# Kernel optimization log

Measured on AMD Instinct MI355X. Metric: run time of the kernel, lower is better.

The kernel has to match this reference:

```python
import jax, jax.numpy as jnp
import numpy as np

DIM = 180
HEADS = 6
WH, WW = 8, 8
MLP_HIDDEN = 720
EPS = 1e-5


def _rel_pos_index(wh, ww):
    ch = np.arange(wh)
    cw = np.arange(ww)
    coords = np.stack(np.meshgrid(ch, cw, indexing='ij'))  # [2, wh, ww]
    cf = coords.reshape(2, -1)                              # [2, N]
    rc = cf[:, :, None] - cf[:, None, :]                    # [2, N, N]
    rc = rc.transpose(1, 2, 0).astype(np.int64)             # [N, N, 2]
    rc[..., 0] += wh - 1
    rc[..., 1] += ww - 1
    rc[..., 0] *= 2 * ww - 1
    return rc.sum(-1)                                       # [N, N]


REL_IDX = jnp.asarray(_rel_pos_index(WH, WW))


def setup_inputs() -> dict:
    key = jax.random.key(0)
    ks = jax.random.split(key, 16)
    B, H, W = 8, 128, 128
    C = DIM
    s = lambda k, shape, sc=0.02: jax.random.normal(k, shape, jnp.float32) * sc
    return {
        'x': jax.random.normal(ks[0], (B, H * W, C), jnp.float32),
        'norm1_w': jnp.ones((C,), jnp.float32),
        'norm1_b': jnp.zeros((C,), jnp.float32),
        'qkv_w': s(ks[1], (C, 3 * C)),
        'qkv_b': jnp.zeros((3 * C,), jnp.float32),
        'rel_bias_table': s(ks[2], ((2 * WH - 1) * (2 * WW - 1), HEADS)),
        'proj_w': s(ks[3], (C, C)),
        'proj_b': jnp.zeros((C,), jnp.float32),
        'norm2_w': jnp.ones((C,), jnp.float32),
        'norm2_b': jnp.zeros((C,), jnp.float32),
        'fc1_w': s(ks[4], (C, MLP_HIDDEN)),
        'fc1_b': jnp.zeros((MLP_HIDDEN,), jnp.float32),
        'fc2_w': s(ks[5], (MLP_HIDDEN, C)),
        'fc2_b': jnp.zeros((C,), jnp.float32),
        'H': H,
        'W': W,
    }


def _layernorm(x, w, b):
    mu = jnp.mean(x, axis=-1, keepdims=True)
    var = jnp.var(x, axis=-1, keepdims=True)
    return (x - mu) * jax.lax.rsqrt(var + EPS) * w + b


def _swin_block(x, H, W, p):
    B, N, C = x.shape
    hd = C // HEADS
    scale = hd ** -0.5

    x1 = _layernorm(x, p['norm1_w'], p['norm1_b'])
    x1 = x1.reshape(B, H, W, C)
    # window partition -> [nW, WH*WW, C]
    x1 = x1.reshape(B, H // WH, WH, W // WW, WW, C).transpose(0, 1, 3, 2, 4, 5)
    nW = B * (H // WH) * (W // WW)
    Nw = WH * WW
    xw = x1.reshape(nW, Nw, C)

    qkv = xw @ p['qkv_w'] + p['qkv_b']                      # [nW, Nw, 3C]
    qkv = qkv.reshape(nW, Nw, 3, HEADS, hd).transpose(2, 0, 3, 1, 4)
    q, k, v = qkv[0], qkv[1], qkv[2]                        # [nW, H, Nw, hd]

    bias = p['rel_bias_table'][REL_IDX.reshape(-1)].reshape(Nw, Nw, HEADS)
    bias = bias.transpose(2, 0, 1)                          # [H, Nw, Nw]

    attn = jnp.einsum('whqd,whkd->whqk', q * scale, k) + bias[None]
    attn = jax.nn.softmax(attn, axis=-1)
    o = jnp.einsum('whqk,whkd->whqd', attn, v)              # [nW, H, Nw, hd]
    o = o.transpose(0, 2, 1, 3).reshape(nW, Nw, C)
    o = o @ p['proj_w'] + p['proj_b']

    # window reverse -> [B, H, W, C]
    o = o.reshape(B, H // WH, W // WW, WH, WW, C).transpose(0, 1, 3, 2, 4, 5)
    o = o.reshape(B, N, C)

    x1 = o + x
    x2 = _layernorm(x1, p['norm2_w'], p['norm2_b'])
    x2 = jax.nn.gelu(x2 @ p['fc1_w'] + p['fc1_b'], approximate=False) @ p['fc2_w'] + p['fc2_b']
    return x2 + x1


def reference(x, norm1_w, norm1_b, qkv_w, qkv_b, rel_bias_table, proj_w, proj_b,
              norm2_w, norm2_b, fc1_w, fc1_b, fc2_w, fc2_b, H, W):
    p = dict(norm1_w=norm1_w, norm1_b=norm1_b, qkv_w=qkv_w, qkv_b=qkv_b,
             rel_bias_table=rel_bias_table, proj_w=proj_w, proj_b=proj_b,
             norm2_w=norm2_w, norm2_b=norm2_b, fc1_w=fc1_w, fc1_b=fc1_b,
             fc2_w=fc2_w, fc2_b=fc2_b)
    return _swin_block(x, H, W, p)
```

## Files before the change

### kernel.cpp

```cpp
#include <hip/hip_runtime.h>
#include <hip/hip_bf16.h>

typedef __hip_bfloat16 bf16;
typedef __attribute__((ext_vector_type(8))) short short8;
typedef __attribute__((ext_vector_type(4))) short short4v;
typedef __attribute__((ext_vector_type(4))) float f32x4;

#define C_DIM 180
#define CPAD  192
#define NHEAD 6
#define HD    30
#define HID   720
#define HPAD  768
#define QKVW  576
#define LN_EPS 1e-5f
#define IMG_TOK 16384
#define QSCALE 0.18257418583505536f

static __device__ __forceinline__ bf16 f2bf(float f) { return __float2bfloat16(f); }
static __device__ __forceinline__ float bf2f(bf16 v) { return __bfloat162float(v); }
static __device__ __forceinline__ short bfbits(float f) {
    bf16 b = __float2bfloat16(f); return *reinterpret_cast<short*>(&b);
}
static __device__ __forceinline__ float gelu_tanh(float v) {
    float u = 0.7978845608f * (v + 0.044715f * v * v * v);
    float e = __expf(2.f * u);
    return 0.5f * v * (2.f - 2.f / (e + 1.f));
}
static __device__ __forceinline__ float gelu_sig(float v) {
    float e = __expf(-1.702f * v);
    return v * __builtin_amdgcn_rcpf(1.f + e);
}

__global__ __launch_bounds__(256) void prep_w(const float* __restrict__ w, bf16* __restrict__ bt,
                                              int K, int N, int Kpad, int Npad) {
    int idx = blockIdx.x * 256 + threadIdx.x;
    if (idx >= Kpad * Npad) return;
    int k = idx % Kpad, n = idx / Kpad;
    float v = (k < K && n < N) ? w[(long)k * N + n] : 0.f;
    bt[idx] = f2bf(v);
}

__global__ __launch_bounds__(256) void prep_wqkv(const float* __restrict__ w, bf16* __restrict__ bt) {
    int idx = blockIdx.x * 256 + threadIdx.x;
    if (idx >= QKVW * CPAD) return;
    int k = idx % CPAD, c = idx / CPAD;
    int mat = c / 192, rem = c % 192;
    int hh = rem >> 5, dd = rem & 31;
    float v = 0.f;
    if (dd < HD && k < C_DIM) {
        v = w[(long)k * 540 + mat * 180 + hh * 30 + dd];
        if (mat == 0) v *= QSCALE;
    }
    bt[idx] = f2bf(v);
}
__global__ __launch_bounds__(256) void prep_bqkv(const float* __restrict__ b, float* __restrict__ bp) {
    int c = blockIdx.x * 256 + threadIdx.x;
    if (c >= QKVW) return;
    int mat = c / 192, rem = c % 192;
    int hh = rem >> 5, dd = rem & 31;
    float v = 0.f;
    if (dd < HD) {
        v = b[mat * 180 + hh * 30 + dd];
        if (mat == 0) v *= QSCALE;
    }
    bp[c] = v;
}

__global__ __launch_bounds__(256) void prep_f1b(const float* __restrict__ b, float* __restrict__ bp) {
    int i = blockIdx.x * 256 + threadIdx.x;
    if (i < HPAD) bp[i] = (i < HID) ? b[i] : 0.f;
}

__global__ __launch_bounds__(256) void prep_bias(const float* __restrict__ tbl,
                                                 float* __restrict__ bias_frag) {
    int idx = blockIdx.x * 256 + threadIdx.x;
    if (idx >= 6144) return;
    int lane = idx & 63;
    int fj = (idx >> 6) & 3;
    int fi = (idx >> 8) & 3;
    int h  = idx >> 10;
    int g = lane >> 4, l15 = lane & 15;
    int kk = fj * 16 + l15;
    int rk = kk >> 3, ck = kk & 7;
    #pragma unroll
    for (int r = 0; r < 4; ++r) {
        int q = fi * 16 + g * 4 + r;
        int rq = q >> 3, cq = q & 7;
        int bidx = (rq - rk + 7) * 15 + (cq - ck + 7);
        bias_frag[idx * 4 + r] = tbl[bidx * NHEAD + h];
    }
}

__global__ __launch_bounds__(256) void ln_kernel(const float* __restrict__ x,
                                                 const float* __restrict__ w,
                                                 const float* __restrict__ b,
                                                 bf16* __restrict__ out, int M) {
    int wave = threadIdx.x >> 6;
    int lane = threadIdx.x & 63;
    long row = (long)blockIdx.x * 4 + wave;
    if (row >= M) return;
    const float* xr = x + row * C_DIM;
    float e0 = xr[lane];
    float e1 = xr[lane + 64];
    float e2 = (lane < C_DIM - 128) ? xr[lane + 128] : 0.f;
    float s  = e0 + e1 + e2;
    float ss = e0*e0 + e1*e1 + e2*e2;
    #pragma unroll
    for (int off = 32; off > 0; off >>= 1) {
        s  += __shfl_xor(s,  off);
        ss += __shfl_xor(ss, off);
    }
    float mean = s * (1.f / C_DIM);
    float var  = ss * (1.f / C_DIM) - mean * mean;
    float rs   = rsqrtf(var + LN_EPS);
    bf16* orow = out + row * CPAD;
    orow[lane]      = f2bf((e0 - mean) * rs * w[lane]      + b[lane]);
    orow[lane + 64] = f2bf((e1 - mean) * rs * w[lane + 64] + b[lane + 64]);
    if (lane < C_DIM - 128)
        orow[lane + 128] = f2bf((e2 - mean) * rs * w[lane + 128] + b[lane + 128]);
    if (lane < CPAD - C_DIM)
        orow[C_DIM + lane] = f2bf(0.f);
}

#define GLL16(gp, lp) \
    __builtin_amdgcn_global_load_lds((const __attribute__((address_space(1))) unsigned int*)(gp), \
                                     (__attribute__((address_space(3))) unsigned int*)(lp), 16, 0, 0)

template<int DO_GELU, int OUT_MODE>
__global__ __launch_bounds__(256) void mfma_gemm(
    const bf16* __restrict__ A, int lda,
    const bf16* __restrict__ Bt,
    const float* __restrict__ bias,
    const float* __restrict__ resid, int nres,
    void* __restrict__ out, int ldo, int nstore,
    int Kpad, int P)
{
    __shared__ __align__(16) short smem[128 * 64 + 64 * 64];
    short* As = smem;
    short* Bs = smem + 128 * 64;
    int tid  = threadIdx.x;
    int lane = tid & 63;
    int wave = tid >> 6;
    int wm = wave >> 1, wn = wave & 1;
    int g4 = lane >> 4, l15 = lane & 15;

    int flat = blockIdx.x;
    int grp  = flat / (8 * P);
    int rem  = flat - grp * 8 * P;
    int p    = rem >> 3;
    long m0  = (long)(grp * 8 + (rem & 7)) * 128;
    int  n0  = p * 64;

    f32x4 acc[4][2] = {};

    int nkt = Kpad >> 6;
    for (int kt = 0; kt < nkt; ++kt) {
        int k0 = kt << 6;
        #pragma unroll
        for (int i = 0; i < 4; ++i) {
            int f = i * 256 + tid;
            int r = f >> 3, c = f & 7;
            const bf16* gp = A + (m0 + r) * (long)lda + k0 + ((c ^ (r & 7)) << 3);
            GLL16(gp, &As[(i * 256 + (wave << 6)) * 8]);
        }
        #pragma unroll
        for (int i = 0; i < 2; ++i) {
            int f = i * 256 + tid;
            int r = f >> 3, c = f & 7;
            const bf16* gp = Bt + (n0 + r) * (long)Kpad + k0 + ((c ^ (r & 7)) << 3);
            GLL16(gp, &Bs[(i * 256 + (wave << 6)) * 8]);
        }
        __syncthreads();
        #pragma unroll
        for (int ks = 0; ks < 2; ++ks) {
            short8 af[4], bfr[2];
            #pragma unroll
            for (int fi = 0; fi < 4; ++fi) {
                int r  = wm * 64 + fi * 16 + l15;
                int ch = ks * 4 + g4;
                af[fi] = *(const short8*)&As[r * 64 + ((ch ^ (r & 7)) << 3)];
            }
            #pragma unroll
            for (int fj = 0; fj < 2; ++fj) {
                int r  = wn * 32 + fj * 16 + l15;
                int ch = ks * 4 + g4;
                bfr[fj] = *(const short8*)&Bs[r * 64 + ((ch ^ (r & 7)) << 3)];
            }
            #pragma unroll
            for (int fi = 0; fi < 4; ++fi)
                #pragma unroll
                for (int fj = 0; fj < 2; ++fj)
                    acc[fi][fj] = __builtin_amdgcn_mfma_f32_16x16x32_bf16(af[fi], bfr[fj], acc[fi][fj], 0, 0, 0);
        }
        __syncthreads();
    }

    if (OUT_MODE == 0) {
        short* Cs = smem;
        #pragma unroll
        for (int fi = 0; fi < 4; ++fi)
            #pragma unroll
            for (int fj = 0; fj < 2; ++fj) {
                int col = wn * 32 + fj * 16 + l15;
                float bv = (n0 + col < nstore) ? bias[n0 + col] : 0.f;
                #pragma unroll
                for (int rg = 0; rg < 4; ++rg) {
                    int row = wm * 64 + fi * 16 + g4 * 4 + rg;
                    float v = acc[fi][fj][rg] + bv;
                    if (DO_GELU) v = gelu_tanh(v);
                    Cs[row * 72 + col] = bfbits(v);
                }
            }
        __syncthreads();
        #pragma unroll
        for (int i = 0; i < 4; ++i) {
            int t = i * 256 + tid;
            int row = t >> 3, c8 = t & 7;
            short8 v = *(const short8*)&Cs[row * 72 + c8 * 8];
            *(short8*)((bf16*)out + (m0 + row) * (long)ldo + n0 + c8 * 8) = v;
        }
    } else {
        float* Cf = (float*)smem;
        int ncols = nstore - n0; if (ncols > 64) ncols = 64;
        int cpr = ncols >> 2;
        #pragma unroll
        for (int hh = 0; hh < 2; ++hh) {
            if (wm == hh) {
                #pragma unroll
                for (int fi = 0; fi < 4; ++fi)
                    #pragma unroll
                    for (int fj = 0; fj < 2; ++fj) {
                        int col = wn * 32 + fj * 16 + l15;
                        float bv = (n0 + col < nstore) ? bias[n0 + col] : 0.f;
                        #pragma unroll
                        for (int rg = 0; rg < 4; ++rg) {
                            int lrow = fi * 16 + g4 * 4 + rg;
                            Cf[lrow * 68 + col] = acc[fi][fj][rg] + bv;
                        }
                    }
            }
            __syncthreads();
            for (int t = tid; t < 64 * cpr; t += 256) {
                int row = t / cpr, cc = (t - row * cpr) * 4;
                long grow = m0 + hh * 64 + row;
                f32x4 v = *(const f32x4*)&Cf[row * 68 + cc];
                if (resid) {
                    f32x4 rv = *(const f32x4*)(resid + grow * (long)nres + n0 + cc);
                    v += rv;
                }
                *(f32x4*)((float*)out + grow * (long)ldo + n0 + cc) = v;
            }
            __syncthreads();
        }
    }
}

template<int DO_GELU>
__global__ __launch_bounds__(512) void mfma_gemm128(
    const bf16* __restrict__ A, int lda,
    const bf16* __restrict__ Bt,
    const float* __restrict__ bias,
    bf16* __restrict__ out, int ldo,
    int Kpad, int P)
{
    __shared__ __align__(16) short smem[128 * 64 + 128 * 64];
    short* As = smem;
    short* Bs = smem + 128 * 64;
    int tid  = threadIdx.x;
    int lane = tid & 63;
    int wave = tid >> 6;
    int wm = wave >> 1, wn = wave & 1;
    int g4 = lane >> 4, l15 = lane & 15;

    int flat = blockIdx.x;
    int grp  = flat / (8 * P);
    int rem  = flat - grp * 8 * P;
    int p    = rem >> 3;
    long m0  = (long)(grp * 8 + (rem & 7)) * 128;
    int  n0  = p * 128;

    f32x4 acc[2][4] = {};

    int nkt = Kpad >> 6;
    for (int kt = 0; kt < nkt; ++kt) {
        int k0 = kt << 6;
        #pragma unroll
        for (int i = 0; i < 2; ++i) {
            int f = i * 512 + tid;
            int r = f >> 3, c = f & 7;
            const bf16* gp = A + (m0 + r) * (long)lda + k0 + ((c ^ (r & 7)) << 3);
            GLL16(gp, &As[(i * 512 + (wave << 6)) * 8]);
        }
        #pragma unroll
        for (int i = 0; i < 2; ++i) {
            int f = i * 512 + tid;
            int r = f >> 3, c = f & 7;
            const bf16* gp = Bt + (n0 + r) * (long)Kpad + k0 + ((c ^ (r & 7)) << 3);
            GLL16(gp, &Bs[(i * 512 + (wave << 6)) * 8]);
        }
        __syncthreads();
        #pragma unroll
        for (int ks = 0; ks < 2; ++ks) {
            short8 af[2], bfr[4];
            #pragma unroll
            for (int fi = 0; fi < 2; ++fi) {
                int r  = wm * 32 + fi * 16 + l15;
                int ch = ks * 4 + g4;
                af[fi] = *(const short8*)&As[r * 64 + ((ch ^ (r & 7)) << 3)];
            }
            #pragma unroll
            for (int fj = 0; fj < 4; ++fj) {
                int r  = wn * 64 + fj * 16 + l15;
                int ch = ks * 4 + g4;
                bfr[fj] = *(const short8*)&Bs[r * 64 + ((ch ^ (r & 7)) << 3)];
            }
            #pragma unroll
            for (int fi = 0; fi < 2; ++fi)
                #pragma unroll
                for (int fj = 0; fj < 4; ++fj)
                    acc[fi][fj] = __builtin_amdgcn_mfma_f32_16x16x32_bf16(af[fi], bfr[fj], acc[fi][fj], 0, 0, 0);
        }
        __syncthreads();
    }

    short* Cs = smem;
    #pragma unroll
    for (int fi = 0; fi < 2; ++fi)
        #pragma unroll
        for (int fj = 0; fj < 4; ++fj) {
            int col = wn * 64 + fj * 16 + l15;
            float bv = bias[n0 + col];
            #pragma unroll
            for (int rg = 0; rg < 4; ++rg) {
                int row = wm * 32 + fi * 16 + g4 * 4 + rg;
                float v = acc[fi][fj][rg] + bv;
                if (DO_GELU) v = gelu_sig(v);
                int ch = (col >> 3) ^ (row & 7);
                Cs[row * 128 + (ch << 3) + (col & 7)] = bfbits(v);
            }
        }
    __syncthreads();
    #pragma unroll
    for (int i = 0; i < 4; ++i) {
        int t = i * 512 + tid;
        int row = t >> 4, c16 = t & 15;
        short8 v = *(const short8*)&Cs[row * 128 + ((c16 ^ (row & 7)) << 3)];
        *(short8*)(out + (m0 + row) * (long)ldo + n0 + c16 * 8) = v;
    }
}

__global__ __launch_bounds__(384, 3) void attn_mfma(
    const bf16* __restrict__ qkv,
    const float* __restrict__ bias_frag,
    bf16* __restrict__ o)
{
    __shared__ __align__(16) short lds[6 * 4096];
    int tid  = threadIdx.x;
    int wave = tid >> 6;
    int lane = tid & 63;
    int h = wave;
    int w = blockIdx.x;
    int b = w >> 8, rem = w & 255;
    int wi = rem >> 4, wj = rem & 15;
    long base = (long)b * IMG_TOK + wi * 8 * 128 + wj * 8;
    int g = lane >> 4, l15 = lane & 15;

    short* Vt = &lds[wave * 4096];
    short* Ph = &lds[wave * 4096 + 2048];

    short8 qf[4], kf[4];
    #pragma unroll
    for (int fi = 0; fi < 4; ++fi) {
        int q = fi * 16 + l15;
        long t = base + (q >> 3) * 128 + (q & 7);
        const bf16* rowp = qkv + t * QKVW + h * 32 + g * 8;
        qf[fi] = *(const short8*)(rowp);
        kf[fi] = *(const short8*)(rowp + 192);
    }

    {
        int t = lane;
        const bf16* vp = qkv + (base + (t >> 3) * 128 + (t & 7)) * QKVW + 384 + h * 32;
        short8 v0 = *(const short8*)(vp);
        short8 v1 = *(const short8*)(vp + 8);
        short8 v2 = *(const short8*)(vp + 16);
        short8 v3 = *(const short8*)(vp + 24);
        int ct = t >> 3, t7 = t & 7;
        #pragma unroll
        for (int d = 0; d < 8; ++d)  Vt[d * 64 + ((ct ^ d) << 3) + t7] = v0[d];
        #pragma unroll
        for (int d = 8; d < 16; ++d) Vt[d * 64 + ((ct ^ (d & 7)) << 3) + t7] = v1[d - 8];
        #pragma unroll
        for (int d = 16; d < 24; ++d) Vt[d * 64 + ((ct ^ (d & 7)) << 3) + t7] = v2[d - 16];
        #pragma unroll
        for (int d = 24; d < 32; ++d) Vt[d * 64 + ((ct ^ (d & 7)) << 3) + t7] = v3[d - 24];
    }

    f32x4 S[4][4];
    #pragma unroll
    for (int fi = 0; fi < 4; ++fi)
        #pragma unroll
        for (int fj = 0; fj < 4; ++fj)
            S[fi][fj] = *(const f32x4*)(bias_frag + (((h * 4 + fi) * 4 + fj) * 64 + lane) * 4);
    #pragma unroll
    for (int fi = 0; fi < 4; ++fi)
        #pragma unroll
        for (int fj = 0; fj < 4; ++fj)
            S[fi][fj] = __builtin_amdgcn_mfma_f32_16x16x32_bf16(qf[fi], kf[fj], S[fi][fj], 0, 0, 0);

    f32x4 mrow[4], lsum[4];
    #pragma unroll
    for (int fi = 0; fi < 4; ++fi) {
        f32x4 a = S[fi][0], c = S[fi][2];
        #pragma unroll
        for (int cc = 0; cc < 4; ++cc) {
            a[cc] = fmaxf(a[cc], S[fi][1][cc]);
            c[cc] = fmaxf(c[cc], S[fi][3][cc]);
            a[cc] = fmaxf(a[cc], c[cc]);
        }
        mrow[fi] = a;
    }
    #pragma unroll
    for (int mask = 1; mask <= 8; mask <<= 1)
        #pragma unroll
        for (int fi = 0; fi < 4; ++fi)
            #pragma unroll
            for (int cc = 0; cc < 4; ++cc)
                mrow[fi][cc] = fmaxf(mrow[fi][cc], __shfl_xor(mrow[fi][cc], mask));
    #pragma unroll
    for (int fi = 0; fi < 4; ++fi)
        #pragma unroll
        for (int fj = 0; fj < 4; ++fj)
            #pragma unroll
            for (int cc = 0; cc < 4; ++cc)
                S[fi][fj][cc] = __expf(S[fi][fj][cc] - mrow[fi][cc]);
    #pragma unroll
    for (int fi = 0; fi < 4; ++fi) {
        f32x4 a = S[fi][0] + S[fi][1];
        f32x4 c = S[fi][2] + S[fi][3];
        lsum[fi] = a + c;
    }
    #pragma unroll
    for (int mask = 1; mask <= 8; mask <<= 1)
        #pragma unroll
        for (int fi = 0; fi < 4; ++fi)
            #pragma unroll
            for (int cc = 0; cc < 4; ++cc)
                lsum[fi][cc] += __shfl_xor(lsum[fi][cc], mask);

    f32x4 O[4][2] = {};
    #pragma unroll
    for (int ks = 0; ks < 2; ++ks) {
        #pragma unroll
        for (int fi = 0; fi < 4; ++fi)
            #pragma unroll
            for (int f2 = 0; f2 < 2; ++f2) {
                int fj = ks * 2 + f2;
                int kh = f2 * 16 + l15;
                #pragma unroll
                for (int r = 0; r < 4; ++r) {
                    int q = fi * 16 + g * 4 + r;
                    int c = (kh >> 3) ^ r ^ g;
                    Ph[q * 32 + (c << 3) + (kh & 7)] = bfbits(S[fi][fj][r]);
                }
            }
        short8 vf[2];
        #pragma unroll
        for (int f2 = 0; f2 < 2; ++f2) {
            int d = f2 * 16 + l15;
            int cv = (ks * 4 + g) ^ (d & 7);
            vf[f2] = *(const short8*)&Vt[d * 64 + (cv << 3)];
        }
        #pragma unroll
        for (int fi = 0; fi < 4; ++fi) {
            int q = fi * 16 + l15;
            int cr = g ^ (q & 3) ^ ((q >> 2) & 3);
            short8 pf = *(const short8*)&Ph[q * 32 + (cr << 3)];
            #pragma unroll
            for (int f2 = 0; f2 < 2; ++f2)
                O[fi][f2] = __builtin_amdgcn_mfma_f32_16x16x32_bf16(pf, vf[f2], O[fi][f2], 0, 0, 0);
        }
    }

    #pragma unroll
    for (int fi = 0; fi < 4; ++fi) {
        f32x4 inv;
        #pragma unroll
        for (int cc = 0; cc < 4; ++cc) inv[cc] = 1.f / lsum[fi][cc];
        #pragma unroll
        for (int r = 0; r < 4; ++r) {
            int q = fi * 16 + g * 4 + r;
            long t = base + (q >> 3) * 128 + (q & 7);
            bf16* op = o + t * CPAD + h * HD;
            op[l15] = f2bf(O[fi][0][r] * inv[r]);
            if (l15 < HD - 16)
                op[16 + l15] = f2bf(O[fi][1][r] * inv[r]);
        }
    }
    if (h == 0) {
        long t = base + (lane >> 3) * 128 + (lane & 7);
        bf16* op = o + t * CPAD + C_DIM;
        short4v z4 = {0, 0, 0, 0};
        short8  z8 = {0, 0, 0, 0, 0, 0, 0, 0};
        *(short4v*)(op) = z4;
        *(short8*)(op + 4) = z8;
    }
}

extern "C" void kernel_launch(void* const* d_in, const int* in_sizes, int n_in,
                              void* d_out, int out_size, void* d_ws, size_t ws_size,
                              hipStream_t stream) {
    const float* x    = (const float*)d_in[0];
    const float* n1w  = (const float*)d_in[1];
    const float* n1b  = (const float*)d_in[2];
    const float* qkvw = (const float*)d_in[3];
    const float* qkvb = (const float*)d_in[4];
    const float* tbl  = (const float*)d_in[5];
    const float* pw   = (const float*)d_in[6];
    const float* pb   = (const float*)d_in[7];
    const float* n2w  = (const float*)d_in[8];
    const float* n2b  = (const float*)d_in[9];
    const float* f1w  = (const float*)d_in[10];
    const float* f1b  = (const float*)d_in[11];
    const float* f2w  = (const float*)d_in[12];
    const float* f2b  = (const float*)d_in[13];

    auto al = [](size_t b) { return (b + 255) & ~(size_t)255; };
    char* base = (char*)d_ws;
    size_t off = 0;
    auto alloc = [&](size_t bytes) -> char* { char* p = base + off; off += al(bytes); return p; };

    bf16* wqp  = (bf16*)alloc((size_t)QKVW * CPAD * 2);
    bf16* wp   = (bf16*)alloc((size_t)192 * 192 * 2);
    bf16* wf1  = (bf16*)alloc((size_t)768 * 192 * 2);
    bf16* wf2  = (bf16*)alloc((size_t)192 * 768 * 2);
    float* bfr = (float*)alloc((size_t)6144 * 4 * 4);
    float* f1bp = (float*)alloc((size_t)HPAD * 4);
    float* qbp  = (float*)alloc((size_t)QKVW * 4);
    size_t woff = off;

    size_t r1_per = al((size_t)IMG_TOK * HPAD * 2);
    size_t r2_per = al((size_t)IMG_TOK * CPAD * 2);
    size_t r3_per = al((size_t)IMG_TOK * C_DIM * 4);
    size_t per_img = r1_per + r2_per + r3_per;
    int g = 8;
    while (g > 1 && woff + per_img * (size_t)g > ws_size) g >>= 1;
    int nchunks = 8 / g;
    long Mc = (long)IMG_TOK * g;
    int nm = (int)(Mc / 128);

    bf16*  R1 = (bf16*)(base + woff);
    bf16*  R2 = (bf16*)(base + woff + r1_per * g);
    float* R3 = (float*)(base + woff + (r1_per + r2_per) * g);

    prep_wqkv<<<(QKVW * CPAD + 255) / 256, 256, 0, stream>>>(qkvw, wqp);
    prep_bqkv<<<(QKVW + 255) / 256, 256, 0, stream>>>(qkvb, qbp);
    prep_w<<<(192 * 192 + 255) / 256, 256, 0, stream>>>(pw, wp, 180, 180, 192, 192);
    prep_w<<<(768 * 192 + 255) / 256, 256, 0, stream>>>(f1w, wf1, 180, 720, 192, 768);
    prep_w<<<(192 * 768 + 255) / 256, 256, 0, stream>>>(f2w, wf2, 720, 180, 768, 192);
    prep_bias<<<(6144 + 255) / 256, 256, 0, stream>>>(tbl, bfr);
    prep_f1b<<<(HPAD + 255) / 256, 256, 0, stream>>>(f1b, f1bp);

    for (int ci = 0; ci < nchunks; ++ci) {
        const float* xc   = x + (size_t)ci * Mc * C_DIM;
        float*       outc = (float*)d_out + (size_t)ci * Mc * C_DIM;

        ln_kernel<<<Mc / 4, 256, 0, stream>>>(xc, n1w, n1b, R2, (int)Mc);
        mfma_gemm<0, 0><<<dim3(nm * 9), 256, 0, stream>>>(
            R2, CPAD, wqp, qbp, nullptr, 0, R1, QKVW, QKVW, CPAD, 9);
        attn_mfma<<<dim3(256 * g), 384, 0, stream>>>(R1, bfr, R2);
        mfma_gemm<0, 1><<<dim3(nm * 3), 256, 0, stream>>>(
            R2, CPAD, wp, pb, xc, 180, R3, 180, 180, CPAD, 3);
        ln_kernel<<<Mc / 4, 256, 0, stream>>>(R3, n2w, n2b, R2, (int)Mc);
        mfma_gemm128<1><<<dim3(nm * 6), 512, 0, stream>>>(
            R2, CPAD, wf1, f1bp, R1, HPAD, CPAD, 6);
        mfma_gemm<0, 1><<<dim3(nm * 3), 256, 0, stream>>>(
            R1, HPAD, wf2, f2b, R3, 180, outc, 180, 180, HPAD, 3);
    }
}
```

Baseline: 458.9 us.

## Add full-width 128x192 GEMM tile for proj and fc2 output GEMMs

Adds a new 512-thread GEMM kernel where each block computes a 128-row by full 192-column output tile, replacing the 128x64 tiles that needed three column blocks per row strip. The A tile is loaded once per row strip instead of three times, which cuts redundant global/LDS traffic for the proj and fc2 GEMMs (fc2 has K=768, so this matters most there). The fused bias + residual epilogue is now done in four 32-row phases through LDS. The trade-off is a third as many blocks, a larger LDS footprint (40 KB), and more accumulator registers, which may lower occupancy. The old templated GEMM is reduced to the bf16-output path, and the unused tanh GELU helper is removed.

```diff
diff --git a/kernel.cpp b/kernel.cpp
--- a/kernel.cpp
+++ b/kernel.cpp
@@ -21,11 +21,6 @@
 static __device__ __forceinline__ float bf2f(bf16 v) { return __bfloat162float(v); }
 static __device__ __forceinline__ short bfbits(float f) {
     bf16 b = __float2bfloat16(f); return *reinterpret_cast<short*>(&b);
-}
-static __device__ __forceinline__ float gelu_tanh(float v) {
-    float u = 0.7978845608f * (v + 0.044715f * v * v * v);
-    float e = __expf(2.f * u);
-    return 0.5f * v * (2.f - 2.f / (e + 1.f));
 }
 static __device__ __forceinline__ float gelu_sig(float v) {
     float e = __expf(-1.702f * v);
@@ -127,13 +122,11 @@
     __builtin_amdgcn_global_load_lds((const __attribute__((address_space(1))) unsigned int*)(gp), \
                                      (__attribute__((address_space(3))) unsigned int*)(lp), 16, 0, 0)
 
-template<int DO_GELU, int OUT_MODE>
 __global__ __launch_bounds__(256) void mfma_gemm(
     const bf16* __restrict__ A, int lda,
     const bf16* __restrict__ Bt,
     const float* __restrict__ bias,
-    const float* __restrict__ resid, int nres,
-    void* __restrict__ out, int ldo, int nstore,
+    bf16* __restrict__ out, int ldo, int nstore,
     int Kpad, int P)
 {
     __shared__ __align__(16) short smem[128 * 64 + 64 * 64];
@@ -196,63 +189,123 @@
         __syncthreads();
     }
 
-    if (OUT_MODE == 0) {
-        short* Cs = smem;
-        #pragma unroll
-        for (int fi = 0; fi < 4; ++fi)
-            #pragma unroll
-            for (int fj = 0; fj < 2; ++fj) {
-                int col = wn * 32 + fj * 16 + l15;
-                float bv = (n0 + col < nstore) ? bias[n0 + col] : 0.f;
+    short* Cs = smem;
+    #pragma unroll
+    for (int fi = 0; fi < 4; ++fi)
+        #pragma unroll
+        for (int fj = 0; fj < 2; ++fj) {
+            int col = wn * 32 + fj * 16 + l15;
+            float bv = (n0 + col < nstore) ? bias[n0 + col] : 0.f;
+            #pragma unroll
+            for (int rg = 0; rg < 4; ++rg) {
+                int row = wm * 64 + fi * 16 + g4 * 4 + rg;
+                Cs[row * 72 + col] = bfbits(acc[fi][fj][rg] + bv);
+            }
+        }
+    __syncthreads();
+    #pragma unroll
+    for (int i = 0; i < 4; ++i) {
+        int t = i * 256 + tid;
+        int row = t >> 3, c8 = t & 7;
+        short8 v = *(const short8*)&Cs[row * 72 + c8 * 8];
+        *(short8*)(out + (m0 + row) * (long)ldo + n0 + c8 * 8) = v;
+    }
+}
+
+__global__ __launch_bounds__(512) void mfma_gemm192(
+    const bf16* __restrict__ A, int lda,
+    const bf16* __restrict__ Bt,
+    const float* __restrict__ bias,
+    const float* __restrict__ resid, int nres,
+    float* __restrict__ out, int ldo, int nstore,
+    int Kpad)
+{
+    __shared__ __align__(16) short smem[128 * 64 + 192 * 64];
+    short* As = smem;
+    short* Bs = smem + 128 * 64;
+    int tid  = threadIdx.x;
+    int lane = tid & 63;
+    int wave = tid >> 6;
+    int wm = wave >> 1, wn = wave & 1;
+    int g4 = lane >> 4, l15 = lane & 15;
+
+    int flat = blockIdx.x;
+    long m0  = (long)flat * 128;
+
+    f32x4 acc[2][6] = {};
+
+    int nkt = Kpad >> 6;
+    for (int kt = 0; kt < nkt; ++kt) {
+        int k0 = kt << 6;
+        #pragma unroll
+        for (int i = 0; i < 2; ++i) {
+            int f = i * 512 + tid;
+            int r = f >> 3, c = f & 7;
+            const bf16* gp = A + (m0 + r) * (long)lda + k0 + ((c ^ (r & 7)) << 3);
+            GLL16(gp, &As[(i * 512 + (wave << 6)) * 8]);
+        }
+        #pragma unroll
+        for (int i = 0; i < 3; ++i) {
+            int f = i * 512 + tid;
+            int r = f >> 3, c = f & 7;
+            const bf16* gp = Bt + r * (long)Kpad + k0 + ((c ^ (r & 7)) << 3);
+            GLL16(gp, &Bs[(i * 512 + (wave << 6)) * 8]);
+        }
+        __syncthreads();
+        #pragma unroll
+        for (int ks = 0; ks < 2; ++ks) {
+            short8 af[2], bfr[6];
+            #pragma unroll
+            for (int fi = 0; fi < 2; ++fi) {
+                int r  = wm * 32 + fi * 16 + l15;
+                int ch = ks * 4 + g4;
+                af[fi] = *(const short8*)&As[r * 64 + ((ch ^ (r & 7)) << 3)];
+            }
+            #pragma unroll
+            for (int fj = 0; fj < 6; ++fj) {
+                int r  = wn * 96 + fj * 16 + l15;
+                int ch = ks * 4 + g4;
+                bfr[fj] = *(const short8*)&Bs[r * 64 + ((ch ^ (r & 7)) << 3)];
+            }
+            #pragma unroll
+            for (int fi = 0; fi < 2; ++fi)
                 #pragma unroll
-                for (int rg = 0; rg < 4; ++rg) {
-                    int row = wm * 64 + fi * 16 + g4 * 4 + rg;
-                    float v = acc[fi][fj][rg] + bv;
-                    if (DO_GELU) v = gelu_tanh(v);
-                    Cs[row * 72 + col] = bfbits(v);
+                for (int fj = 0; fj < 6; ++fj)
+                    acc[fi][fj] = __builtin_amdgcn_mfma_f32_16x16x32_bf16(af[fi], bfr[fj], acc[fi][fj], 0, 0, 0);
+        }
+        __syncthreads();
+    }
+
+    float* Cf = (float*)smem;
+    int cpr = nstore >> 2;
+    #pragma unroll
+    for (int ph = 0; ph < 4; ++ph) {
+        if (wm == ph) {
+            #pragma unroll
+            for (int fi = 0; fi < 2; ++fi)
+                #pragma unroll
+                for (int fj = 0; fj < 6; ++fj) {
+                    int col = wn * 96 + fj * 16 + l15;
+                    float bv = (col < nstore) ? bias[col] : 0.f;
+                    #pragma unroll
+                    for (int rg = 0; rg < 4; ++rg) {
+                        int lrow = fi * 16 + g4 * 4 + rg;
+                        Cf[lrow * 196 + col] = acc[fi][fj][rg] + bv;
+                    }
                 }
-            }
-        __syncthreads();
-        #pragma unroll
-        for (int i = 0; i < 4; ++i) {
-            int t = i * 256 + tid;
-            int row = t >> 3, c8 = t & 7;
-            short8 v = *(const short8*)&Cs[row * 72 + c8 * 8];
-            *(short8*)((bf16*)out + (m0 + row) * (long)ldo + n0 + c8 * 8) = v;
-        }
-    } else {
-        float* Cf = (float*)smem;
-        int ncols = nstore - n0; if (ncols > 64) ncols = 64;
-        int cpr = ncols >> 2;
-        #pragma unroll
-        for (int hh = 0; hh < 2; ++hh) {
-            if (wm == hh) {
-                #pragma unroll
-                for (int fi = 0; fi < 4; ++fi)
-                    #pragma unroll
-                    for (int fj = 0; fj < 2; ++fj) {
-                        int col = wn * 32 + fj * 16 + l15;
-                        float bv = (n0 + col < nstore) ? bias[n0 + col] : 0.f;
-                        #pragma unroll
-                        for (int rg = 0; rg < 4; ++rg) {
-                            int lrow = fi * 16 + g4 * 4 + rg;
-                            Cf[lrow * 68 + col] = acc[fi][fj][rg] + bv;
-                        }
-                    }
-            }
-            __syncthreads();
-            for (int t = tid; t < 64 * cpr; t += 256) {
-                int row = t / cpr, cc = (t - row * cpr) * 4;
-                long grow = m0 + hh * 64 + row;
-                f32x4 v = *(const f32x4*)&Cf[row * 68 + cc];
-                if (resid) {
-                    f32x4 rv = *(const f32x4*)(resid + grow * (long)nres + n0 + cc);
-                    v += rv;
-                }
-                *(f32x4*)((float*)out + grow * (long)ldo + n0 + cc) = v;
-            }
-            __syncthreads();
-        }
+        }
+        __syncthreads();
+        for (int t = tid; t < 32 * cpr; t += 512) {
+            int row = t / cpr, cc = (t - row * cpr) * 4;
+            long grow = m0 + ph * 32 + row;
+            f32x4 v = *(const f32x4*)&Cf[row * 196 + cc];
+            if (resid) {
+                f32x4 rv = *(const f32x4*)(resid + grow * (long)nres + cc);
+                v += rv;
+            }
+            *(f32x4*)(out + grow * (long)ldo + cc) = v;
+        }
+        __syncthreads();
     }
 }
 
@@ -567,15 +620,15 @@
         float*       outc = (float*)d_out + (size_t)ci * Mc * C_DIM;
 
         ln_kernel<<<Mc / 4, 256, 0, stream>>>(xc, n1w, n1b, R2, (int)Mc);
-        mfma_gemm<0, 0><<<dim3(nm * 9), 256, 0, stream>>>(
-            R2, CPAD, wqp, qbp, nullptr, 0, R1, QKVW, QKVW, CPAD, 9);
+        mfma_gemm<<<dim3(nm * 9), 256, 0, stream>>>(
+            R2, CPAD, wqp, qbp, R1, QKVW, QKVW, CPAD, 9);
         attn_mfma<<<dim3(256 * g), 384, 0, stream>>>(R1, bfr, R2);
-        mfma_gemm<0, 1><<<dim3(nm * 3), 256, 0, stream>>>(
-            R2, CPAD, wp, pb, xc, 180, R3, 180, 180, CPAD, 3);
+        mfma_gemm192<<<dim3(nm), 512, 0, stream>>>(
+            R2, CPAD, wp, pb, xc, 180, R3, 180, 180, CPAD);
         ln_kernel<<<Mc / 4, 256, 0, stream>>>(R3, n2w, n2b, R2, (int)Mc);
         mfma_gemm128<1><<<dim3(nm * 6), 512, 0, stream>>>(
             R2, CPAD, wf1, f1bp, R1, HPAD, CPAD, 6);
-        mfma_gemm<0, 1><<<dim3(nm * 3), 256, 0, stream>>>(
-            R1, HPAD, wf2, f2b, R3, 180, outc, 180, 180, HPAD, 3);
-    }
-}
+        mfma_gemm192<<<dim3(nm), 512, 0, stream>>>(
+            R1, HPAD, wf2, f2b, R3, 180, outc, 180, 180, HPAD);
+    }
+}
```

New measurement: 445.1 us, median of 2. 1.03x faster.
